# Performance work log

Measured on AMD Instinct MI355X. Metric: run time of the kernel, lower is better.

Reference implementation:

```python
import jax, jax.numpy as jnp
import numpy as np

N = 8192
F_IN = 512
F_OUT = 64
ALPHA = 0.2  # LeakyReLU negative slope
MASK_VAL = -9e15


def setup_inputs() -> dict:
    key = jax.random.key(0)
    k1, k2, k3, k4, k5 = jax.random.split(key, 5)
    x = jax.random.normal(k1, (N, F_IN), dtype=jnp.float32)
    adj = jax.random.randint(k2, (N, N), 0, 2, dtype=jnp.int32)
    # params: W uniform(-stdv, stdv) per reset_parameters, A xavier-ish
    stdv = 1.0 / np.sqrt(F_OUT)
    W = jax.random.uniform(k3, (F_IN, F_OUT), dtype=jnp.float32, minval=-stdv, maxval=stdv)
    bias = jax.random.uniform(k4, (F_OUT,), dtype=jnp.float32, minval=-stdv, maxval=stdv)
    A = jax.random.normal(k5, (2 * F_OUT, 1), dtype=jnp.float32) * 0.1
    return {"x": x, "adj": adj, "W": W, "bias": bias, "A": A}


def reference(x, adj, W, bias, A):
    # Wh: [N, F_OUT]
    Wh = x @ W
    # e_ij = leakyrelu([Wh_i || Wh_j] @ A) == leakyrelu(Wh_i @ a1 + Wh_j @ a2)
    # (mathematically identical to the N x N x 2F concat, without materializing it)
    a1 = A[:F_OUT, 0]  # [F_OUT]
    a2 = A[F_OUT:, 0]  # [F_OUT]
    s1 = Wh @ a1  # [N]
    s2 = Wh @ a2  # [N]
    e = jax.nn.leaky_relu(s1[:, None] + s2[None, :], negative_slope=ALPHA)  # [N, N]
    masked = jnp.where(adj > 0, e, MASK_VAL)
    attention = jax.nn.softmax(masked, axis=1)  # [N, N]
    # dropout p=0.0 -> identity
    out = attention @ Wh + bias  # [N, F_OUT]
    return out
```

## Files before the change

### kernel.cpp

```cpp
#include <hip/hip_runtime.h>

#define NN 8192
#define FIN 512
#define FOUT 64
#define LRELU_ALPHA 0.2f
#define LOG2E 1.4426950408889634f

typedef __attribute__((ext_vector_type(4))) float f32x4;
typedef __attribute__((ext_vector_type(4))) int i32x4;
typedef __attribute__((ext_vector_type(8))) __bf16 bf16x8;

#if __has_builtin(__builtin_amdgcn_exp2f)
#define EXP2F(x) __builtin_amdgcn_exp2f(x)
#else
#define EXP2F(x) exp2f(x)
#endif

__global__ __launch_bounds__(256) void gat_wh(
    const float* __restrict__ x, const float* __restrict__ W,
    const float* __restrict__ A,
    __bf16* __restrict__ WhbT, float* __restrict__ s1, float* __restrict__ s2)
{
    const int gid  = blockIdx.x * 256 + threadIdx.x;
    const int row  = gid >> 6;
    const int lane = threadIdx.x & 63;
    const int cg   = lane & 15;
    const int kh   = lane >> 4;

    f32x4 acc = {0.f, 0.f, 0.f, 0.f};
    const float* xrow = x + (size_t)row * FIN + kh * 128;
    const float* wcol = W + cg * 4 + (size_t)kh * 128 * FOUT;

    #pragma unroll 4
    for (int k = 0; k < 128; k += 4) {
        f32x4 xv = *reinterpret_cast<const f32x4*>(xrow + k);
        #pragma unroll
        for (int u = 0; u < 4; ++u) {
            f32x4 wv = *reinterpret_cast<const f32x4*>(wcol + (size_t)(k + u) * FOUT);
            acc += xv[u] * wv;
        }
    }

    #pragma unroll
    for (int u = 0; u < 4; ++u) {
        acc[u] += __shfl_xor(acc[u], 16);
        acc[u] += __shfl_xor(acc[u], 32);
    }

    f32x4 a1v = *reinterpret_cast<const f32x4*>(A + cg * 4);
    f32x4 a2v = *reinterpret_cast<const f32x4*>(A + FOUT + cg * 4);
    float s1p = acc[0]*a1v[0] + acc[1]*a1v[1] + acc[2]*a1v[2] + acc[3]*a1v[3];
    float s2p = acc[0]*a2v[0] + acc[1]*a2v[1] + acc[2]*a2v[2] + acc[3]*a2v[3];
    #pragma unroll
    for (int off = 1; off < 16; off <<= 1) {
        s1p += __shfl_xor(s1p, off);
        s2p += __shfl_xor(s2p, off);
    }
    if (lane == 0) { s1[row] = s1p; s2[row] = s2p; }

    if (kh == 0) {
        #pragma unroll
        for (int u = 0; u < 4; ++u)
            WhbT[(size_t)(cg * 4 + u) * NN + row] = (__bf16)acc[u];
    }
}

__global__ __launch_bounds__(256) void gat_attn(
    const int* __restrict__ adj, const __bf16* __restrict__ WhbT,
    const float* __restrict__ s1g, const float* __restrict__ s2g,
    const float* __restrict__ bias, float* __restrict__ out)
{
    __shared__ float s2l[NN];
    __shared__ float red[4];
    __shared__ float ol[4][16];
    __shared__ float oacc[4][16][FOUT];

    const int tid  = threadIdx.x;
    const int w    = tid >> 6;
    const int lane = tid & 63;
    const int r    = lane & 15;
    const int q    = lane >> 4;
    const int row0 = blockIdx.x * 16;

    float mx = -3.0e38f;
    for (int i = tid; i < NN / 4; i += 256) {
        f32x4 v = reinterpret_cast<const f32x4*>(s2g)[i];
        v *= LOG2E;
        reinterpret_cast<f32x4*>(s2l)[i] = v;
        mx = fmaxf(mx, fmaxf(fmaxf(v[0], v[1]), fmaxf(v[2], v[3])));
    }
    #pragma unroll
    for (int off = 1; off < 64; off <<= 1)
        mx = fmaxf(mx, __shfl_xor(mx, off));
    if (lane == 0) red[w] = mx;
    __syncthreads();
    const float s2maxl = fmaxf(fmaxf(red[0], red[1]), fmaxf(red[2], red[3]));

    const float s1l = s1g[row0 + r] * LOG2E;
    const float tM  = s1l + s2maxl;
    const float Ml  = fmaxf(tM, LRELU_ALPHA * tM);

    float l = 0.f;
    f32x4 acc0 = {0,0,0,0}, acc1 = {0,0,0,0}, acc2 = {0,0,0,0}, acc3 = {0,0,0,0};

    const int*    adjp = adj + (size_t)(row0 + r) * NN + q * 8;
    const __bf16* wp   = WhbT + q * 8;
    const float*  s2b_ = s2l + q * 8;

    for (int it = 0; it < 32; ++it) {
        const int j0 = (w << 11) + (it << 6);
        #pragma unroll
        for (int c = 0; c < 2; ++c) {
            const int jc = j0 + (c << 5);
            i32x4 av0 = *reinterpret_cast<const i32x4*>(adjp + jc);
            i32x4 av1 = *reinterpret_cast<const i32x4*>(adjp + jc + 4);
            bf16x8 b0 = *reinterpret_cast<const bf16x8*>(wp + (size_t)(0 * 16 + r) * NN + jc);
            bf16x8 b1 = *reinterpret_cast<const bf16x8*>(wp + (size_t)(1 * 16 + r) * NN + jc);
            bf16x8 b2 = *reinterpret_cast<const bf16x8*>(wp + (size_t)(2 * 16 + r) * NN + jc);
            bf16x8 b3 = *reinterpret_cast<const bf16x8*>(wp + (size_t)(3 * 16 + r) * NN + jc);
            f32x4 s2a = *reinterpret_cast<const f32x4*>(s2b_ + jc);
            f32x4 s2c = *reinterpret_cast<const f32x4*>(s2b_ + jc + 4);

            bf16x8 af;
            float ps = 0.f;
            #pragma unroll
            for (int i = 0; i < 4; ++i) {
                float t0 = s1l + s2a[i];
                float g0 = fmaxf(t0, LRELU_ALPHA * t0) - Ml;
                g0 = (av0[i] > 0) ? g0 : -3.0e38f;
                float p0 = EXP2F(g0);
                ps += p0;
                af[i] = (__bf16)p0;
                float t1 = s1l + s2c[i];
                float g1 = fmaxf(t1, LRELU_ALPHA * t1) - Ml;
                g1 = (av1[i] > 0) ? g1 : -3.0e38f;
                float p1 = EXP2F(g1);
                ps += p1;
                af[i + 4] = (__bf16)p1;
            }
            l += ps;
            acc0 = __builtin_amdgcn_mfma_f32_16x16x32_bf16(af, b0, acc0, 0, 0, 0);
            acc1 = __builtin_amdgcn_mfma_f32_16x16x32_bf16(af, b1, acc1, 0, 0, 0);
            acc2 = __builtin_amdgcn_mfma_f32_16x16x32_bf16(af, b2, acc2, 0, 0, 0);
            acc3 = __builtin_amdgcn_mfma_f32_16x16x32_bf16(af, b3, acc3, 0, 0, 0);
        }
    }

    l += __shfl_xor(l, 16);
    l += __shfl_xor(l, 32);
    if (lane < 16) ol[w][lane] = l;
    #pragma unroll
    for (int reg = 0; reg < 4; ++reg) {
        oacc[w][q * 4 + reg][0 * 16 + r] = acc0[reg];
        oacc[w][q * 4 + reg][1 * 16 + r] = acc1[reg];
        oacc[w][q * 4 + reg][2 * 16 + r] = acc2[reg];
        oacc[w][q * 4 + reg][3 * 16 + r] = acc3[reg];
    }
    __syncthreads();

    for (int o = tid; o < 16 * FOUT; o += 256) {
        const int rr = o >> 6;
        const int f  = o & 63;
        const float L = ol[0][rr] + ol[1][rr] + ol[2][rr] + ol[3][rr];
        const float O = oacc[0][rr][f] + oacc[1][rr][f] + oacc[2][rr][f] + oacc[3][rr][f];
        out[(size_t)(row0 + rr) * FOUT + f] = O / L + bias[f];
    }
}

extern "C" void kernel_launch(void* const* d_in, const int* in_sizes, int n_in,
                              void* d_out, int out_size, void* d_ws, size_t ws_size,
                              hipStream_t stream)
{
    const float* x    = (const float*)d_in[0];
    const int*   adj  = (const int*)d_in[1];
    const float* W    = (const float*)d_in[2];
    const float* bias = (const float*)d_in[3];
    const float* A    = (const float*)d_in[4];
    float* out = (float*)d_out;

    char* ws = (char*)d_ws;
    __bf16* WhbT = (__bf16*)ws;
    float*  s1   = (float*)(ws + (size_t)FOUT * NN * sizeof(__bf16));
    float*  s2   = s1 + NN;

    gat_wh<<<dim3(NN / 4), dim3(256), 0, stream>>>(x, W, A, WhbT, s1, s2);
    gat_attn<<<dim3(NN / 16), dim3(256), 0, stream>>>(adj, WhbT, s1, s2, bias, out);
}
```

Baseline: 436.1 us.

## Split attention columns into strips across blocks and merge partial sums

Splits the attention kernel's key dimension into four column strips, so each block handles a 16-row by 2048-column tile. This launches four times as many blocks and improves occupancy and load balance across CUs. Each block writes partial numerators and denominators to workspace, and a new merge kernel sums them, divides, and adds bias. The cost is an extra launch, partial-sum traffic, and every block still reading the full s2 vector to find the global max.

```diff
diff --git a/kernel.cpp b/kernel.cpp
--- a/kernel.cpp
+++ b/kernel.cpp
@@ -5,6 +5,9 @@
 #define FOUT 64
 #define LRELU_ALPHA 0.2f
 #define LOG2E 1.4426950408889634f
+#define NSTRIP 4
+#define STRIPC (NN / NSTRIP)
+#define WAVEC  (STRIPC / 4)
 
 typedef __attribute__((ext_vector_type(4))) float f32x4;
 typedef __attribute__((ext_vector_type(4))) int i32x4;
@@ -68,9 +71,9 @@
 __global__ __launch_bounds__(256) void gat_attn(
     const int* __restrict__ adj, const __bf16* __restrict__ WhbT,
     const float* __restrict__ s1g, const float* __restrict__ s2g,
-    const float* __restrict__ bias, float* __restrict__ out)
-{
-    __shared__ float s2l[NN];
+    float* __restrict__ Opart, float* __restrict__ lpart)
+{
+    __shared__ float s2l[STRIPC];
     __shared__ float red[4];
     __shared__ float ol[4][16];
     __shared__ float oacc[4][16][FOUT];
@@ -80,14 +83,19 @@
     const int lane = tid & 63;
     const int r    = lane & 15;
     const int q    = lane >> 4;
-    const int row0 = blockIdx.x * 16;
+    const int rowblk  = blockIdx.x >> 2;
+    const int cs      = blockIdx.x & 3;
+    const int row0    = rowblk * 16;
+    const int colbase = cs * STRIPC;
 
     float mx = -3.0e38f;
     for (int i = tid; i < NN / 4; i += 256) {
         f32x4 v = reinterpret_cast<const f32x4*>(s2g)[i];
         v *= LOG2E;
-        reinterpret_cast<f32x4*>(s2l)[i] = v;
         mx = fmaxf(mx, fmaxf(fmaxf(v[0], v[1]), fmaxf(v[2], v[3])));
+        const int li = i - cs * (STRIPC / 4);
+        if ((unsigned)li < (unsigned)(STRIPC / 4))
+            reinterpret_cast<f32x4*>(s2l)[li] = v;
     }
     #pragma unroll
     for (int off = 1; off < 64; off <<= 1)
@@ -103,12 +111,12 @@
     float l = 0.f;
     f32x4 acc0 = {0,0,0,0}, acc1 = {0,0,0,0}, acc2 = {0,0,0,0}, acc3 = {0,0,0,0};
 
-    const int*    adjp = adj + (size_t)(row0 + r) * NN + q * 8;
-    const __bf16* wp   = WhbT + q * 8;
-    const float*  s2b_ = s2l + q * 8;
-
-    for (int it = 0; it < 32; ++it) {
-        const int j0 = (w << 11) + (it << 6);
+    const int*    adjp = adj + (size_t)(row0 + r) * NN + colbase + (w * WAVEC) + q * 8;
+    const __bf16* wp   = WhbT + colbase + (w * WAVEC) + q * 8;
+    const float*  s2b_ = s2l + (w * WAVEC) + q * 8;
+
+    for (int it = 0; it < WAVEC / 64; ++it) {
+        const int j0 = it << 6;
         #pragma unroll
         for (int c = 0; c < 2; ++c) {
             const int jc = j0 + (c << 5);
@@ -163,8 +171,30 @@
         const int f  = o & 63;
         const float L = ol[0][rr] + ol[1][rr] + ol[2][rr] + ol[3][rr];
         const float O = oacc[0][rr][f] + oacc[1][rr][f] + oacc[2][rr][f] + oacc[3][rr][f];
-        out[(size_t)(row0 + rr) * FOUT + f] = O / L + bias[f];
-    }
+        Opart[((size_t)cs * NN + row0 + rr) * FOUT + f] = O;
+        if (f == 0) lpart[cs * NN + row0 + rr] = L;
+    }
+}
+
+__global__ __launch_bounds__(256) void gat_merge(
+    const float* __restrict__ Opart, const float* __restrict__ lpart,
+    const float* __restrict__ bias, float* __restrict__ out)
+{
+    const int idx = blockIdx.x * 256 + threadIdx.x;
+    const int row = idx >> 4;
+    const int fg  = idx & 15;
+
+    f32x4 O = {0.f, 0.f, 0.f, 0.f};
+    float L = 0.f;
+    #pragma unroll
+    for (int cs = 0; cs < NSTRIP; ++cs) {
+        O += *reinterpret_cast<const f32x4*>(Opart + ((size_t)cs * NN + row) * FOUT + fg * 4);
+        L += lpart[cs * NN + row];
+    }
+    const f32x4 bv = *reinterpret_cast<const f32x4*>(bias + fg * 4);
+    const float inv = 1.0f / L;
+    f32x4 res = O * inv + bv;
+    *reinterpret_cast<f32x4*>(out + (size_t)row * FOUT + fg * 4) = res;
 }
 
 extern "C" void kernel_launch(void* const* d_in, const int* in_sizes, int n_in,
@@ -179,10 +209,13 @@
     float* out = (float*)d_out;
 
     char* ws = (char*)d_ws;
-    __bf16* WhbT = (__bf16*)ws;
-    float*  s1   = (float*)(ws + (size_t)FOUT * NN * sizeof(__bf16));
-    float*  s2   = s1 + NN;
+    __bf16* WhbT  = (__bf16*)ws;
+    float*  s1    = (float*)(ws + (size_t)FOUT * NN * sizeof(__bf16));
+    float*  s2    = s1 + NN;
+    float*  Opart = s2 + NN;
+    float*  lpart = Opart + (size_t)NSTRIP * NN * FOUT;
 
     gat_wh<<<dim3(NN / 4), dim3(256), 0, stream>>>(x, W, A, WhbT, s1, s2);
-    gat_attn<<<dim3(NN / 16), dim3(256), 0, stream>>>(adj, WhbT, s1, s2, bias, out);
-}
+    gat_attn<<<dim3(512 * NSTRIP), dim3(256), 0, stream>>>(adj, WhbT, s1, s2, Opart, lpart);
+    gat_merge<<<dim3(NN * 16 / 256), dim3(256), 0, stream>>>(Opart, lpart, bias, out);
+}
```

Result: no change. 441.9 us (+1.3%).
